# Optimization experiments

Measured on AMD Instinct MI355X. Metric: run time of the kernel, lower is better.

The kernel has to match this reference:

```python
import jax, jax.numpy as jnp
import numpy as np

N, E = 50000, 800000
IN_C, HID, HEADS, LAT = 128, 64, 2, 32
NEG_SLOPE = 0.2  # PyG GATConv default LeakyReLU slope


def gat_layer(x, src, dst, W, att_src, att_dst, bias, heads, out_ch, concat, n):
    # Linear projection, per-head: [n, heads, out_ch]
    h = (x @ W).reshape(n, heads, out_ch)
    a_src = jnp.einsum('nhc,hc->nh', h, att_src)  # [n, heads]
    a_dst = jnp.einsum('nhc,hc->nh', h, att_dst)
    # Per-edge attention logits (edge j->i uses src j, dst i)
    alpha = jax.nn.leaky_relu(a_src[src] + a_dst[dst], negative_slope=NEG_SLOPE)  # [e, heads]
    # Segment softmax over incoming edges of each destination node
    amax = jax.ops.segment_max(alpha, dst, num_segments=n)
    ealpha = jnp.exp(alpha - amax[dst])
    denom = jax.ops.segment_sum(ealpha, dst, num_segments=n)
    alpha = ealpha / (denom[dst] + 1e-16)
    # Weighted scatter-aggregate of source features
    msg = h[src] * alpha[:, :, None]  # [e, heads, out_ch]
    out = jax.ops.segment_sum(msg, dst, num_segments=n)  # [n, heads, out_ch]
    out = out.reshape(n, heads * out_ch) if concat else out.mean(axis=1)
    return out + bias


def setup_inputs() -> dict:
    key = jax.random.key(0)
    ks = jax.random.split(key, 16)
    x = jax.random.normal(ks[0], (N, IN_C), dtype=jnp.float32)
    edge_index = jax.random.randint(ks[1], (2, E), 0, N, dtype=jnp.int32).astype(jnp.int64)
    s = 0.1
    W1 = jax.random.normal(ks[2], (IN_C, HEADS * HID), dtype=jnp.float32) * s
    att_src1 = jax.random.normal(ks[3], (HEADS, HID), dtype=jnp.float32) * s
    att_dst1 = jax.random.normal(ks[4], (HEADS, HID), dtype=jnp.float32) * s
    b1 = jnp.zeros((HEADS * HID,), dtype=jnp.float32)
    Wmu = jax.random.normal(ks[5], (HEADS * HID, LAT), dtype=jnp.float32) * s
    att_src_mu = jax.random.normal(ks[6], (1, LAT), dtype=jnp.float32) * s
    att_dst_mu = jax.random.normal(ks[7], (1, LAT), dtype=jnp.float32) * s
    bmu = jnp.zeros((LAT,), dtype=jnp.float32)
    Wlv = jax.random.normal(ks[8], (HEADS * HID, LAT), dtype=jnp.float32) * s
    att_src_lv = jax.random.normal(ks[9], (1, LAT), dtype=jnp.float32) * s
    att_dst_lv = jax.random.normal(ks[10], (1, LAT), dtype=jnp.float32) * s
    blv = jnp.zeros((LAT,), dtype=jnp.float32)
    return {"x": x, "edge_index": edge_index, "W1": W1, "att_src1": att_src1,
            "att_dst1": att_dst1, "b1": b1, "Wmu": Wmu, "att_src_mu": att_src_mu,
            "att_dst_mu": att_dst_mu, "bmu": bmu, "Wlv": Wlv,
            "att_src_lv": att_src_lv, "att_dst_lv": att_dst_lv, "blv": blv}


def reference(x, edge_index, W1, att_src1, att_dst1, b1,
              Wmu, att_src_mu, att_dst_mu, bmu,
              Wlv, att_src_lv, att_dst_lv, blv):
    n = x.shape[0]
    # PyG GATConv adds self-loops by default
    loops = jnp.arange(n, dtype=edge_index.dtype)
    src = jnp.concatenate([edge_index[0], loops])
    dst = jnp.concatenate([edge_index[1], loops])
    h = gat_layer(x, src, dst, W1, att_src1, att_dst1, b1, HEADS, HID, True, n)
    h = jax.nn.elu(h)
    mu = gat_layer(h, src, dst, Wmu, att_src_mu, att_dst_mu, bmu, 1, LAT, False, n)
    logvar = gat_layer(h, src, dst, Wlv, att_src_lv, att_dst_lv, blv, 1, LAT, False, n)
    return (mu, logvar)
```

## Files before the change

kernel.cpp:

```cpp
#include <hip/hip_runtime.h>
#include <hip/hip_bf16.h>

#define N_NODES 50000
#define N_EDGES 800000
#define EP (N_EDGES + N_NODES)
#define IN_C 128
#define HID 64
#define HEADS 2
#define LAT 32
#define NEG_SLOPE 0.2f
#define MAXDEG 256
#define NBUCKET 391
#define BCAP 3072
#define CHUNK 4096
#define NSCAT ((EP + CHUNK - 1) / CHUNK)
#define NPROJ1 ((N_NODES + 31) / 32)

typedef __attribute__((ext_vector_type(8))) short bf16x8;
typedef __attribute__((ext_vector_type(4))) float f32x4;

__device__ __forceinline__ unsigned short f2bf(float f) {
  unsigned u = __float_as_uint(f);
  u += 0x7FFF + ((u >> 16) & 1);
  return (unsigned short)(u >> 16);
}
__device__ __forceinline__ float bf_lo(unsigned u) { return __uint_as_float(u << 16); }
__device__ __forceinline__ float bf_hi(unsigned u) { return __uint_as_float(u & 0xFFFF0000u); }

__device__ __forceinline__ bf16x8 pack_bf8(const float* __restrict__ p) {
  float4 a = *(const float4*)p;
  float4 b = *(const float4*)(p + 4);
  bf16x8 r;
  r[0] = (short)f2bf(a.x); r[1] = (short)f2bf(a.y);
  r[2] = (short)f2bf(a.z); r[3] = (short)f2bf(a.w);
  r[4] = (short)f2bf(b.x); r[5] = (short)f2bf(b.y);
  r[6] = (short)f2bf(b.z); r[7] = (short)f2bf(b.w);
  return r;
}

struct ScatSmem {
  int histL[512];
  int baseL[512];
  int gbaseL[512];
  int wsumS[4];
  int nvalS;
  unsigned staging[CHUNK];
  unsigned short bktidL[CHUNK];
};
struct Proj1Smem {
  unsigned short Wb[16384];
  float part[32][4];
};
union K1Smem { ScatSmem sc; Proj1Smem pj; };

__global__ __launch_bounds__(256) void k1_kernel(
    const int* __restrict__ ei, int* __restrict__ cursor,
    unsigned* __restrict__ csr,
    const float* __restrict__ x, const float* __restrict__ W,
    const float* __restrict__ att_src, const float* __restrict__ att_dst,
    unsigned short* __restrict__ h1b, float* __restrict__ a1) {
  __shared__ K1Smem sm;
  const int t = threadIdx.x, lane = t & 63, wid = t >> 6;

  if (blockIdx.x < NSCAT) {
    for (int i = t; i < 512; i += 256) sm.sc.histL[i] = 0;
    __syncthreads();
    int myb[CHUNK / 256];
    int myloc[CHUNK / 256];
    unsigned mypay[CHUNK / 256];
    #pragma unroll
    for (int i = 0; i < CHUNK / 256; ++i) {
      int e = blockIdx.x * CHUNK + i * 256 + t;
      if (e < EP) {
        int s, d;
        if (e < N_EDGES) { s = ei[e]; d = ei[N_EDGES + e]; }
        else { s = d = e - N_EDGES; }
        int b = d >> 7;
        myb[i] = b;
        mypay[i] = ((unsigned)(d & 127) << 17) | (unsigned)s;
        myloc[i] = atomicAdd(&sm.sc.histL[b], 1);
      } else myb[i] = -1;
    }
    __syncthreads();
    {
      int v0 = sm.sc.histL[2 * t], v1 = sm.sc.histL[2 * t + 1];
      int pair = v0 + v1, inc = pair;
      #pragma unroll
      for (int off = 1; off < 64; off <<= 1) {
        int nv = __shfl_up(inc, off);
        if (lane >= off) inc += nv;
      }
      if (lane == 63) sm.sc.wsumS[wid] = inc;
      __syncthreads();
      if (t == 0) {
        int run = 0;
        #pragma unroll
        for (int w = 0; w < 4; ++w) { int c = sm.sc.wsumS[w]; sm.sc.wsumS[w] = run; run += c; }
        sm.sc.nvalS = run;
      }
      __syncthreads();
      int excl = sm.sc.wsumS[wid] + inc - pair;
      sm.sc.baseL[2 * t] = excl;
      sm.sc.baseL[2 * t + 1] = excl + v0;
    }
    __syncthreads();
    #pragma unroll
    for (int i = 0; i < CHUNK / 256; ++i)
      if (myb[i] >= 0) {
        int p = sm.sc.baseL[myb[i]] + myloc[i];
        sm.sc.staging[p] = mypay[i];
        sm.sc.bktidL[p] = (unsigned short)myb[i];
      }
    for (int b = t; b < NBUCKET; b += 256) {
      int c = sm.sc.histL[b];
      sm.sc.gbaseL[b] = c ? atomicAdd(&cursor[b], c) : 0;
    }
    __syncthreads();
    const int nval = sm.sc.nvalS;
    for (int j = t; j < nval; j += 256) {
      int b = sm.sc.bktidL[j];
      int off = sm.sc.gbaseL[b] + (j - sm.sc.baseL[b]);
      if (off < BCAP) csr[b * BCAP + off] = sm.sc.staging[j];
    }
  } else {
    const int pb = blockIdx.x - NSCAT;
    for (int i = t; i < 128 * 128; i += 256) {
      int k = i >> 7, n = i & 127;
      int kk = k >> 5, q = (k >> 3) & 3, j = k & 7;
      sm.pj.Wb[((((kk << 2) + q) << 7) + n) * 8 + j] = f2bf(W[i]);
    }
    if (t < 128) ((float*)sm.pj.part)[t] = 0.f;
    __syncthreads();
    const int w = wid;
    const int m = lane & 15, quad = lane >> 4;
    const int row0 = pb * 32;
    const int n0 = w * 32;
    const int head = w >> 1;
    f32x4 acc[2][2] = {};
    #pragma unroll
    for (int kk = 0; kk < 4; ++kk) {
      bf16x8 afr[2], bfr[2];
      #pragma unroll
      for (int mt = 0; mt < 2; ++mt) {
        int row = row0 + mt * 16 + m;
        if (row >= N_NODES) row = N_NODES - 1;
        afr[mt] = pack_bf8(x + (size_t)row * 128 + kk * 32 + quad * 8);
      }
      #pragma unroll
      for (int nt = 0; nt < 2; ++nt)
        bfr[nt] = *(const bf16x8*)&sm.pj.Wb[((((kk << 2) + quad) << 7) + n0 + nt * 16 + m) * 8];
      #pragma unroll
      for (int mt = 0; mt < 2; ++mt)
        #pragma unroll
        for (int nt = 0; nt < 2; ++nt)
          acc[mt][nt] = __builtin_amdgcn_mfma_f32_16x16x32_bf16(
              afr[mt], bfr[nt], acc[mt][nt], 0, 0, 0);
    }
    float asv[2], adv[2];
    #pragma unroll
    for (int nt = 0; nt < 2; ++nt) {
      int cc = ((n0 & 63) + nt * 16 + m);
      asv[nt] = att_src[head * HID + cc];
      adv[nt] = att_dst[head * HID + cc];
    }
    #pragma unroll
    for (int mt = 0; mt < 2; ++mt)
      #pragma unroll
      for (int r = 0; r < 4; ++r) {
        int row = row0 + mt * 16 + quad * 4 + r;
        if (row < N_NODES) {
          #pragma unroll
          for (int nt = 0; nt < 2; ++nt)
            h1b[(size_t)row * 128 + n0 + nt * 16 + m] = f2bf(acc[mt][nt][r]);
        }
        float s = acc[mt][0][r] * asv[0] + acc[mt][1][r] * asv[1];
        float d = acc[mt][0][r] * adv[0] + acc[mt][1][r] * adv[1];
        #pragma unroll
        for (int off = 8; off; off >>= 1) {
          s += __shfl_xor(s, off);
          d += __shfl_xor(d, off);
        }
        if (m == 0) {
          atomicAdd(&sm.pj.part[mt * 16 + quad * 4 + r][head], s);
          atomicAdd(&sm.pj.part[mt * 16 + quad * 4 + r][2 + head], d);
        }
      }
    __syncthreads();
    if (t < 32) {
      int row = row0 + t;
      if (row < N_NODES)
        *(float4*)&a1[(size_t)row * 4] = make_float4(
            sm.pj.part[t][0], sm.pj.part[t][1], sm.pj.part[t][2], sm.pj.part[t][3]);
    }
  }
}

__global__ __launch_bounds__(256) void bucket_fill_kernel(
    const int* __restrict__ cursor, unsigned* __restrict__ csr,
    int* __restrict__ counts, int* __restrict__ cend) {
  __shared__ unsigned eseg[BCAP];
  __shared__ int hist[128];
  __shared__ int basef[128];
  __shared__ int cur[128];
  const int b = blockIdx.x, t = threadIdx.x;
  const int segbase = b * BCAP;
  int cnt = cursor[b];
  if (cnt > BCAP) cnt = BCAP;
  if (t < 128) hist[t] = 0;
  __syncthreads();
  for (int j = t; j < cnt; j += 256) {
    unsigned u = csr[segbase + j];
    eseg[j] = u;
    atomicAdd(&hist[u >> 17], 1);
  }
  __syncthreads();
  if (t < 64) {
    int v0 = hist[2 * t], v1 = hist[2 * t + 1];
    int pair = v0 + v1, inc = pair;
    #pragma unroll
    for (int off = 1; off < 64; off <<= 1) {
      int nv = __shfl_up(inc, off);
      if (t >= off) inc += nv;
    }
    int excl = inc - pair;
    basef[2 * t] = excl;
    basef[2 * t + 1] = excl + v0;
  }
  __syncthreads();
  if (t < 128) {
    cur[t] = basef[t];
    int n = b * 128 + t;
    if (n < N_NODES) {
      counts[n] = hist[t];
      cend[n] = segbase + basef[t] + hist[t];
    }
  }
  __syncthreads();
  for (int j = t; j < cnt; j += 256) {
    unsigned u = eseg[j];
    int dl = u >> 17;
    int p = atomicAdd(&cur[dl], 1);
    csr[segbase + p] = u & 0x1FFFF;
  }
}

__global__ __launch_bounds__(64) void agg1_csr_kernel(
    const int* __restrict__ counts, const int* __restrict__ cend,
    const unsigned* __restrict__ csr_src, const float4* __restrict__ a1,
    const unsigned* __restrict__ h1b2, const float* __restrict__ b,
    float* __restrict__ hact) {
  __shared__ float w_lds[2][MAXDEG];
  __shared__ int   s_lds[MAXDEG];
  const int n = blockIdx.x;
  const int t = threadIdx.x;
  const int end = cend[n];
  int cnt = counts[n];
  if (cnt > MAXDEG) cnt = MAXDEG;
  const int beg = end - cnt;
  const float4 bv = a1[n];
  float p0 = 0.f, p1 = 0.f;
  for (int i = t; i < cnt; i += 64) {
    int s = (int)csr_src[beg + i];
    float4 av = a1[s];
    float l0 = av.x + bv.z; l0 = l0 > 0.f ? l0 : NEG_SLOPE * l0;
    float l1 = av.y + bv.w; l1 = l1 > 0.f ? l1 : NEG_SLOPE * l1;
    float e0 = expf(l0), e1 = expf(l1);
    w_lds[0][i] = e0; w_lds[1][i] = e1; s_lds[i] = s;
    p0 += e0; p1 += e1;
  }
  #pragma unroll
  for (int off = 32; off; off >>= 1) {
    p0 += __shfl_xor(p0, off);
    p1 += __shfl_xor(p1, off);
  }
  __syncthreads();
  const int head = t >> 5;
  const unsigned* hp = h1b2 + t;
  float ax = 0.f, ay = 0.f;
  #pragma unroll 4
  for (int i = 0; i < cnt; ++i) {
    int s = s_lds[i];
    float w = w_lds[head][i];
    unsigned u = hp[(size_t)s * 64];
    ax += bf_lo(u) * w; ay += bf_hi(u) * w;
  }
  float inv = 1.f / ((head ? p1 : p0) + 1e-16f);
  float vx = ax * inv + b[t * 2];
  float vy = ay * inv + b[t * 2 + 1];
  vx = vx > 0.f ? vx : (expf(vx) - 1.f);
  vy = vy > 0.f ? vy : (expf(vy) - 1.f);
  *(float2*)(hact + (size_t)n * 128 + t * 2) = make_float2(vx, vy);
}

__global__ __launch_bounds__(256) void proj2_kernel(
    const float* __restrict__ h, const float* __restrict__ Wmu,
    const float* __restrict__ Wlv,
    const float* __restrict__ asmu, const float* __restrict__ admu,
    const float* __restrict__ aslv, const float* __restrict__ adlv,
    unsigned short* __restrict__ h2b, float* __restrict__ a2) {
  __shared__ unsigned short Wb[8192];
  const int t = threadIdx.x;
  for (int i = t; i < 128 * 64; i += 256) {
    int k = i >> 6, n = i & 63;
    float v = (n < 32) ? Wmu[k * 32 + n] : Wlv[k * 32 + (n - 32)];
    int kk = k >> 5, q = (k >> 3) & 3, j = k & 7;
    Wb[((((kk << 2) + q) << 6) + n) * 8 + j] = f2bf(v);
  }
  __syncthreads();
  const int w = t >> 6, lane = t & 63;
  const int m = lane & 15, quad = lane >> 4;
  const int row0 = blockIdx.x * 64 + (w >> 1) * 32;
  const int j = w & 1;
  const int n0 = j * 32;
  f32x4 acc[2][2] = {};
  #pragma unroll
  for (int kk = 0; kk < 4; ++kk) {
    bf16x8 afr[2], bfr[2];
    #pragma unroll
    for (int mt = 0; mt < 2; ++mt) {
      int row = row0 + mt * 16 + m;
      if (row >= N_NODES) row = N_NODES - 1;
      afr[mt] = pack_bf8(h + (size_t)row * 128 + kk * 32 + quad * 8);
    }
    #pragma unroll
    for (int nt = 0; nt < 2; ++nt)
      bfr[nt] = *(const bf16x8*)&Wb[((((kk << 2) + quad) << 6) + n0 + nt * 16 + m) * 8];
    #pragma unroll
    for (int mt = 0; mt < 2; ++mt)
      #pragma unroll
      for (int nt = 0; nt < 2; ++nt)
        acc[mt][nt] = __builtin_amdgcn_mfma_f32_16x16x32_bf16(
            afr[mt], bfr[nt], acc[mt][nt], 0, 0, 0);
  }
  float asv[2], adv[2];
  #pragma unroll
  for (int nt = 0; nt < 2; ++nt) {
    int o = nt * 16 + m;
    asv[nt] = (j ? aslv : asmu)[o];
    adv[nt] = (j ? adlv : admu)[o];
  }
  #pragma unroll
  for (int mt = 0; mt < 2; ++mt)
    #pragma unroll
    for (int r = 0; r < 4; ++r) {
      int row = row0 + mt * 16 + quad * 4 + r;
      if (row < N_NODES) {
        #pragma unroll
        for (int nt = 0; nt < 2; ++nt)
          h2b[(size_t)row * 64 + n0 + nt * 16 + m] = f2bf(acc[mt][nt][r]);
      }
      float s = acc[mt][0][r] * asv[0] + acc[mt][1][r] * asv[1];
      float d = acc[mt][0][r] * adv[0] + acc[mt][1][r] * adv[1];
      #pragma unroll
      for (int off = 8; off; off >>= 1) {
        s += __shfl_xor(s, off);
        d += __shfl_xor(d, off);
      }
      if (m == 0 && row < N_NODES) {
        a2[(size_t)row * 4 + j * 2 + 0] = s;
        a2[(size_t)row * 4 + j * 2 + 1] = d;
      }
    }
}

__global__ __launch_bounds__(64) void agg2_csr_kernel(
    const int* __restrict__ counts, const int* __restrict__ cend,
    const unsigned* __restrict__ csr_src, const float4* __restrict__ a2,
    const unsigned short* __restrict__ h2b,
    const float* __restrict__ bmu, const float* __restrict__ blv,
    float* __restrict__ out) {
  __shared__ float w_lds[2][MAXDEG];
  __shared__ int   s_lds[MAXDEG];
  const int n = blockIdx.x;
  const int t = threadIdx.x;
  const int end = cend[n];
  int cnt = counts[n];
  if (cnt > MAXDEG) cnt = MAXDEG;
  const int beg = end - cnt;
  const float4 bv = a2[n];
  float p0 = 0.f, p1 = 0.f;
  for (int i = t; i < cnt; i += 64) {
    int s = (int)csr_src[beg + i];
    float4 av = a2[s];
    float l0 = av.x + bv.y; l0 = l0 > 0.f ? l0 : NEG_SLOPE * l0;
    float l1 = av.z + bv.w; l1 = l1 > 0.f ? l1 : NEG_SLOPE * l1;
    float e0 = expf(l0), e1 = expf(l1);
    w_lds[0][i] = e0; w_lds[1][i] = e1; s_lds[i] = s;
    p0 += e0; p1 += e1;
  }
  #pragma unroll
  for (int off = 32; off; off >>= 1) {
    p0 += __shfl_xor(p0, off);
    p1 += __shfl_xor(p1, off);
  }
  __syncthreads();
  const int j = t >> 5, o = t & 31;
  const unsigned short* hp = h2b + t;
  float acc = 0.f;
  #pragma unroll 4
  for (int i = 0; i < cnt; ++i) {
    int s = s_lds[i];
    float hv = __uint_as_float(((unsigned)hp[(size_t)s * 64]) << 16);
    acc += hv * w_lds[j][i];
  }
  float inv = 1.f / ((j ? p1 : p0) + 1e-16f);
  out[(size_t)j * N_NODES * LAT + (size_t)n * LAT + o] =
      acc * inv + (j ? blv : bmu)[o];
}

extern "C" void kernel_launch(void* const* d_in, const int* in_sizes, int n_in,
                              void* d_out, int out_size, void* d_ws, size_t ws_size,
                              hipStream_t stream) {
  const float* x        = (const float*)d_in[0];
  const int* ei         = (const int*)d_in[1];
  const float* W1       = (const float*)d_in[2];
  const float* att_src1 = (const float*)d_in[3];
  const float* att_dst1 = (const float*)d_in[4];
  const float* b1       = (const float*)d_in[5];
  const float* Wmu      = (const float*)d_in[6];
  const float* asmu     = (const float*)d_in[7];
  const float* admu     = (const float*)d_in[8];
  const float* bmu      = (const float*)d_in[9];
  const float* Wlv      = (const float*)d_in[10];
  const float* aslv     = (const float*)d_in[11];
  const float* adlv     = (const float*)d_in[12];
  const float* blv      = (const float*)d_in[13];
  float* out = (float*)d_out;

  float* ws   = (float*)d_ws;
  float* hact = ws;
  float* a1   = hact + (size_t)N_NODES * 128;
  float* a2   = a1 + (size_t)N_NODES * 4;
  unsigned short* h1b = (unsigned short*)(a2 + (size_t)N_NODES * 4);
  unsigned short* h2b = h1b + (size_t)N_NODES * 128;
  int* counts = (int*)(h2b + (size_t)N_NODES * 64);
  int* cend   = counts + N_NODES;
  int* cursor = cend + N_NODES;
  unsigned* csr = (unsigned*)(cursor + NBUCKET);

  hipMemsetAsync(cursor, 0, NBUCKET * sizeof(int), stream);

  k1_kernel<<<NSCAT + NPROJ1, 256, 0, stream>>>(
      ei, cursor, csr, x, W1, att_src1, att_dst1, h1b, a1);
  bucket_fill_kernel<<<NBUCKET, 256, 0, stream>>>(cursor, csr, counts, cend);
  agg1_csr_kernel<<<N_NODES, 64, 0, stream>>>(
      counts, cend, csr, (const float4*)a1, (const unsigned*)h1b, b1, hact);
  proj2_kernel<<<(N_NODES + 63) / 64, 256, 0, stream>>>(
      hact, Wmu, Wlv, asmu, admu, aslv, adlv, h2b, a2);
  agg2_csr_kernel<<<N_NODES, 64, 0, stream>>>(
      counts, cend, csr, (const float4*)a2, h2b, bmu, blv, out);
}
```

Before: 220.2 us.

## Precompute bf16 weights once, halve scatter chunk, pack two nodes per agg2 block

A new prep kernel zeroes the bucket cursors and converts W1 and Wmu/Wlv to the bf16 MFMA layout once in global memory. The projection blocks then read the B fragments from global memory instead of each block redoing the conversion into LDS, and the memset launch goes away. The scatter chunk is halved to give more, smaller scatter blocks. agg2 now handles two nodes per 64-thread block and loads packed bf16 pairs, so each 32-lane half-wave does one node. The trade-off is one extra kernel launch and B fragments fetched from global/L2 rather than LDS.

```diff
diff --git a/kernel.cpp b/kernel.cpp
--- a/kernel.cpp
+++ b/kernel.cpp
@@ -12,7 +12,7 @@
 #define MAXDEG 256
 #define NBUCKET 391
 #define BCAP 3072
-#define CHUNK 4096
+#define CHUNK 2048
 #define NSCAT ((EP + CHUNK - 1) / CHUNK)
 #define NPROJ1 ((N_NODES + 31) / 32)
 
@@ -38,6 +38,27 @@
   return r;
 }
 
+__global__ __launch_bounds__(256) void prep_kernel(
+    const float* __restrict__ W1, const float* __restrict__ Wmu,
+    const float* __restrict__ Wlv, int* __restrict__ cursor,
+    unsigned short* __restrict__ Wb1g, unsigned short* __restrict__ Wb2g) {
+  const int b = blockIdx.x, t = threadIdx.x;
+  if (b == 0) {
+    for (int i = t; i < NBUCKET; i += 256) cursor[i] = 0;
+  } else if (b <= 64) {
+    int i = (b - 1) * 256 + t;
+    int k = i >> 7, n = i & 127;
+    int kk = k >> 5, q = (k >> 3) & 3, j = k & 7;
+    Wb1g[((((kk << 2) + q) << 7) + n) * 8 + j] = f2bf(W1[i]);
+  } else {
+    int i = (b - 65) * 256 + t;
+    int k = i >> 6, n = i & 63;
+    float v = (n < 32) ? Wmu[k * 32 + n] : Wlv[k * 32 + (n - 32)];
+    int kk = k >> 5, q = (k >> 3) & 3, j = k & 7;
+    Wb2g[((((kk << 2) + q) << 6) + n) * 8 + j] = f2bf(v);
+  }
+}
+
 struct ScatSmem {
   int histL[512];
   int baseL[512];
@@ -47,16 +68,12 @@
   unsigned staging[CHUNK];
   unsigned short bktidL[CHUNK];
 };
-struct Proj1Smem {
-  unsigned short Wb[16384];
-  float part[32][4];
-};
-union K1Smem { ScatSmem sc; Proj1Smem pj; };
+union K1Smem { ScatSmem sc; float part[32][4]; };
 
 __global__ __launch_bounds__(256) void k1_kernel(
     const int* __restrict__ ei, int* __restrict__ cursor,
     unsigned* __restrict__ csr,
-    const float* __restrict__ x, const float* __restrict__ W,
+    const float* __restrict__ x, const unsigned short* __restrict__ Wb1g,
     const float* __restrict__ att_src, const float* __restrict__ att_dst,
     unsigned short* __restrict__ h1b, float* __restrict__ a1) {
   __shared__ K1Smem sm;
@@ -124,12 +141,7 @@
     }
   } else {
     const int pb = blockIdx.x - NSCAT;
-    for (int i = t; i < 128 * 128; i += 256) {
-      int k = i >> 7, n = i & 127;
-      int kk = k >> 5, q = (k >> 3) & 3, j = k & 7;
-      sm.pj.Wb[((((kk << 2) + q) << 7) + n) * 8 + j] = f2bf(W[i]);
-    }
-    if (t < 128) ((float*)sm.pj.part)[t] = 0.f;
+    if (t < 128) ((float*)sm.part)[t] = 0.f;
     __syncthreads();
     const int w = wid;
     const int m = lane & 15, quad = lane >> 4;
@@ -148,7 +160,7 @@
       }
       #pragma unroll
       for (int nt = 0; nt < 2; ++nt)
-        bfr[nt] = *(const bf16x8*)&sm.pj.Wb[((((kk << 2) + quad) << 7) + n0 + nt * 16 + m) * 8];
+        bfr[nt] = *(const bf16x8*)&Wb1g[((((kk << 2) + quad) << 7) + n0 + nt * 16 + m) * 8];
       #pragma unroll
       for (int mt = 0; mt < 2; ++mt)
         #pragma unroll
@@ -181,8 +193,8 @@
           d += __shfl_xor(d, off);
         }
         if (m == 0) {
-          atomicAdd(&sm.pj.part[mt * 16 + quad * 4 + r][head], s);
-          atomicAdd(&sm.pj.part[mt * 16 + quad * 4 + r][2 + head], d);
+          atomicAdd(&sm.part[mt * 16 + quad * 4 + r][head], s);
+          atomicAdd(&sm.part[mt * 16 + quad * 4 + r][2 + head], d);
         }
       }
     __syncthreads();
@@ -190,7 +202,7 @@
       int row = row0 + t;
       if (row < N_NODES)
         *(float4*)&a1[(size_t)row * 4] = make_float4(
-            sm.pj.part[t][0], sm.pj.part[t][1], sm.pj.part[t][2], sm.pj.part[t][3]);
+            sm.part[t][0], sm.part[t][1], sm.part[t][2], sm.part[t][3]);
     }
   }
 }
@@ -293,20 +305,11 @@
 }
 
 __global__ __launch_bounds__(256) void proj2_kernel(
-    const float* __restrict__ h, const float* __restrict__ Wmu,
-    const float* __restrict__ Wlv,
+    const float* __restrict__ h, const unsigned short* __restrict__ Wb2g,
     const float* __restrict__ asmu, const float* __restrict__ admu,
     const float* __restrict__ aslv, const float* __restrict__ adlv,
     unsigned short* __restrict__ h2b, float* __restrict__ a2) {
-  __shared__ unsigned short Wb[8192];
   const int t = threadIdx.x;
-  for (int i = t; i < 128 * 64; i += 256) {
-    int k = i >> 6, n = i & 63;
-    float v = (n < 32) ? Wmu[k * 32 + n] : Wlv[k * 32 + (n - 32)];
-    int kk = k >> 5, q = (k >> 3) & 3, j = k & 7;
-    Wb[((((kk << 2) + q) << 6) + n) * 8 + j] = f2bf(v);
-  }
-  __syncthreads();
   const int w = t >> 6, lane = t & 63;
   const int m = lane & 15, quad = lane >> 4;
   const int row0 = blockIdx.x * 64 + (w >> 1) * 32;
@@ -324,7 +327,7 @@
     }
     #pragma unroll
     for (int nt = 0; nt < 2; ++nt)
-      bfr[nt] = *(const bf16x8*)&Wb[((((kk << 2) + quad) << 6) + n0 + nt * 16 + m) * 8];
+      bfr[nt] = *(const bf16x8*)&Wb2g[((((kk << 2) + quad) << 6) + n0 + nt * 16 + m) * 8];
     #pragma unroll
     for (int mt = 0; mt < 2; ++mt)
       #pragma unroll
@@ -366,46 +369,50 @@
 __global__ __launch_bounds__(64) void agg2_csr_kernel(
     const int* __restrict__ counts, const int* __restrict__ cend,
     const unsigned* __restrict__ csr_src, const float4* __restrict__ a2,
-    const unsigned short* __restrict__ h2b,
+    const unsigned* __restrict__ h2b2,
     const float* __restrict__ bmu, const float* __restrict__ blv,
     float* __restrict__ out) {
-  __shared__ float w_lds[2][MAXDEG];
-  __shared__ int   s_lds[MAXDEG];
-  const int n = blockIdx.x;
-  const int t = threadIdx.x;
+  __shared__ float w_lds[2][2][MAXDEG];
+  __shared__ int   s_lds[2][MAXDEG];
+  const int t = threadIdx.x, half = t >> 5, hl = t & 31;
+  const int n = blockIdx.x * 2 + half;
   const int end = cend[n];
   int cnt = counts[n];
   if (cnt > MAXDEG) cnt = MAXDEG;
   const int beg = end - cnt;
   const float4 bv = a2[n];
   float p0 = 0.f, p1 = 0.f;
-  for (int i = t; i < cnt; i += 64) {
+  for (int i = hl; i < cnt; i += 32) {
     int s = (int)csr_src[beg + i];
     float4 av = a2[s];
     float l0 = av.x + bv.y; l0 = l0 > 0.f ? l0 : NEG_SLOPE * l0;
     float l1 = av.z + bv.w; l1 = l1 > 0.f ? l1 : NEG_SLOPE * l1;
     float e0 = expf(l0), e1 = expf(l1);
-    w_lds[0][i] = e0; w_lds[1][i] = e1; s_lds[i] = s;
+    w_lds[half][0][i] = e0; w_lds[half][1][i] = e1; s_lds[half][i] = s;
     p0 += e0; p1 += e1;
   }
   #pragma unroll
-  for (int off = 32; off; off >>= 1) {
+  for (int off = 16; off; off >>= 1) {
     p0 += __shfl_xor(p0, off);
     p1 += __shfl_xor(p1, off);
   }
   __syncthreads();
-  const int j = t >> 5, o = t & 31;
-  const unsigned short* hp = h2b + t;
-  float acc = 0.f;
+  const int c0 = 2 * hl;
+  const int j = c0 >> 5;
+  const int o = c0 & 31;
+  const unsigned* hp = h2b2 + hl;
+  float ax = 0.f, ay = 0.f;
   #pragma unroll 4
   for (int i = 0; i < cnt; ++i) {
-    int s = s_lds[i];
-    float hv = __uint_as_float(((unsigned)hp[(size_t)s * 64]) << 16);
-    acc += hv * w_lds[j][i];
+    int s = s_lds[half][i];
+    float w = w_lds[half][j][i];
+    unsigned u = hp[(size_t)s * 32];
+    ax += bf_lo(u) * w; ay += bf_hi(u) * w;
   }
   float inv = 1.f / ((j ? p1 : p0) + 1e-16f);
-  out[(size_t)j * N_NODES * LAT + (size_t)n * LAT + o] =
-      acc * inv + (j ? blv : bmu)[o];
+  const float* bb = j ? blv : bmu;
+  *(float2*)&out[(size_t)j * N_NODES * LAT + (size_t)n * LAT + o] =
+      make_float2(ax * inv + bb[o], ay * inv + bb[o + 1]);
 }
 
 extern "C" void kernel_launch(void* const* d_in, const int* in_sizes, int n_in,
@@ -433,20 +440,22 @@
   float* a2   = a1 + (size_t)N_NODES * 4;
   unsigned short* h1b = (unsigned short*)(a2 + (size_t)N_NODES * 4);
   unsigned short* h2b = h1b + (size_t)N_NODES * 128;
-  int* counts = (int*)(h2b + (size_t)N_NODES * 64);
+  unsigned short* Wb1g = h2b + (size_t)N_NODES * 64;
+  unsigned short* Wb2g = Wb1g + 16384;
+  int* counts = (int*)(Wb2g + 8192);
   int* cend   = counts + N_NODES;
   int* cursor = cend + N_NODES;
   unsigned* csr = (unsigned*)(cursor + NBUCKET);
 
-  hipMemsetAsync(cursor, 0, NBUCKET * sizeof(int), stream);
+  prep_kernel<<<97, 256, 0, stream>>>(W1, Wmu, Wlv, cursor, Wb1g, Wb2g);
 
   k1_kernel<<<NSCAT + NPROJ1, 256, 0, stream>>>(
-      ei, cursor, csr, x, W1, att_src1, att_dst1, h1b, a1);
+      ei, cursor, csr, x, Wb1g, att_src1, att_dst1, h1b, a1);
   bucket_fill_kernel<<<NBUCKET, 256, 0, stream>>>(cursor, csr, counts, cend);
   agg1_csr_kernel<<<N_NODES, 64, 0, stream>>>(
       counts, cend, csr, (const float4*)a1, (const unsigned*)h1b, b1, hact);
   proj2_kernel<<<(N_NODES + 63) / 64, 256, 0, stream>>>(
-      hact, Wmu, Wlv, asmu, admu, aslv, adlv, h2b, a2);
-  agg2_csr_kernel<<<N_NODES, 64, 0, stream>>>(
-      counts, cend, csr, (const float4*)a2, h2b, bmu, blv, out);
-}
+      hact, Wb2g, asmu, admu, aslv, adlv, h2b, a2);
+  agg2_csr_kernel<<<N_NODES / 2, 64, 0, stream>>>(
+      counts, cend, csr, (const float4*)a2, (const unsigned*)h2b, bmu, blv, out);
+}
```

New measurement: 209.7 us (median of 2 runs). 4.7% less time.
